# Performance work log

Measured on AMD Instinct MI355X. Metric: run time of the kernel, lower is better.

Reference implementation:

```python
import jax, jax.numpy as jnp
import numpy as np

B, S, DIM, H = 8, 1024, 1024, 16
HID = 512  # FeedForward default hidden_dim=512 (module passes only dim)
DH = DIM // H
EPS = 1e-5


def setup_inputs() -> dict:
    key = jax.random.key(0)
    ks = jax.random.split(key, 12)
    s = 1.0 / np.sqrt(DIM)
    return {
        "x": jax.random.normal(ks[0], (B, S, DIM), dtype=jnp.float32),
        "Wq": jax.random.normal(ks[1], (DIM, DIM), dtype=jnp.float32) * s,
        "Wk": jax.random.normal(ks[2], (DIM, DIM), dtype=jnp.float32) * s,
        "Wv": jax.random.normal(ks[3], (DIM, DIM), dtype=jnp.float32) * s,
        "Wo": jax.random.normal(ks[4], (DIM, DIM), dtype=jnp.float32) * s,
        "ln1_g": jnp.ones((DIM,), jnp.float32),
        "ln1_b": jnp.zeros((DIM,), jnp.float32),
        "W1": jax.random.normal(ks[5], (DIM, HID), dtype=jnp.float32) * s,
        "b1": jnp.zeros((HID,), jnp.float32),
        "W2": jax.random.normal(ks[6], (HID, DIM), dtype=jnp.float32) * (1.0 / np.sqrt(HID)),
        "b2": jnp.zeros((DIM,), jnp.float32),
        "ln2_g": jnp.ones((DIM,), jnp.float32),
        "ln2_b": jnp.zeros((DIM,), jnp.float32),
    }


def _layer_norm(x, g, b):
    mu = jnp.mean(x, axis=-1, keepdims=True)
    var = jnp.mean(jnp.square(x - mu), axis=-1, keepdims=True)
    return (x - mu) * jax.lax.rsqrt(var + EPS) * g + b


def reference(x, Wq, Wk, Wv, Wo, ln1_g, ln1_b, W1, b1, W2, b2, ln2_g, ln2_b):
    # Multi-head self-attention (dropout = identity at eval)
    def heads(t):  # [B,S,DIM] -> [B,H,S,DH]
        return t.reshape(B, S, H, DH).transpose(0, 2, 1, 3)

    q = heads(x @ Wq)
    k = heads(x @ Wk)
    v = heads(x @ Wv)
    scores = jnp.einsum("bhqd,bhkd->bhqk", q, k) / jnp.sqrt(jnp.float32(DH))
    attn = jax.nn.softmax(scores, axis=-1)
    ctx = jnp.einsum("bhqk,bhkd->bhqd", attn, v)
    ctx = ctx.transpose(0, 2, 1, 3).reshape(B, S, DIM)
    mha = ctx @ Wo

    h = _layer_norm(mha + x, ln1_g, ln1_b)
    ff = jax.nn.relu(h @ W1 + b1) @ W2 + b2
    out = _layer_norm(ff + h, ln2_g, ln2_b)
    return out
```

## Files before the change

### kernel.cpp

```cpp
#include <hip/hip_runtime.h>
#include <cstdint>
#include <cstddef>

#define DEV __device__ __forceinline__

typedef __bf16 bf16x8 __attribute__((ext_vector_type(8)));
typedef __bf16 bf16x4 __attribute__((ext_vector_type(4)));
typedef short  short4v __attribute__((ext_vector_type(4)));
typedef float  f32x4  __attribute__((ext_vector_type(4)));

static constexpr int Bb  = 8;
static constexpr int S   = 1024;
static constexpr int DIM = 1024;
static constexpr int H   = 16;
static constexpr int DH  = 64;
static constexpr int HID = 512;
static constexpr int M   = Bb * S;

DEV uint16_t f2bf(float f) {
  union { float f; uint32_t u; } v; v.f = f;
  uint32_t r = v.u + 0x7fffu + ((v.u >> 16) & 1u);
  return (uint16_t)(r >> 16);
}
DEV float bf2f(uint32_t u) {
  union { uint32_t u; float f; } v; v.u = u << 16;
  return v.f;
}

DEV void gl_lds16(const uint16_t* g, uint16_t* lds) {
  __builtin_amdgcn_global_load_lds(
      (const __attribute__((address_space(1))) void*)g,
      (__attribute__((address_space(3))) void*)lds, 16, 0, 0);
}

DEV bf16x8 ld8(const uint16_t* p) { return *reinterpret_cast<const bf16x8*>(p); }

#if __has_builtin(__builtin_amdgcn_mfma_f32_16x16x16bf16_1k)
DEV f32x4 mfma16(bf16x4 a, bf16x4 b, f32x4 c) {
  return __builtin_amdgcn_mfma_f32_16x16x16bf16_1k(
      __builtin_bit_cast(short4v, a), __builtin_bit_cast(short4v, b), c, 0, 0, 0);
}
#else
DEV f32x4 mfma16(bf16x4 a, bf16x4 b, f32x4 c) {
  asm volatile("v_mfma_f32_16x16x16_bf16 %0, %1, %2, %0" : "+v"(c) : "v"(a), "v"(b));
  return c;
}
#endif

DEV int swz(int row, int col) {
  return row * 64 + (((col >> 3) ^ (row & 7)) << 3) + (col & 7);
}

__global__ __launch_bounds__(256) void prep_all(const float* __restrict__ x,
                                                uint16_t* __restrict__ x16,
                                                const float* __restrict__ Wq,
                                                const float* __restrict__ Wk,
                                                const float* __restrict__ Wv,
                                                const float* __restrict__ Wo,
                                                const float* __restrict__ W1,
                                                const float* __restrict__ W2,
                                                uint16_t* __restrict__ wqkv_t,
                                                uint16_t* __restrict__ wo_t,
                                                uint16_t* __restrict__ w1_t,
                                                uint16_t* __restrict__ w2_t) {
  int bid = blockIdx.x;
  int tid = threadIdx.x;
  if (bid < 4096) {
    int i = (bid * 256 + tid) * 8;
    const float4* p = reinterpret_cast<const float4*>(x + i);
    float4 a = p[0], b = p[1];
    uint4 pk;
    pk.x = (uint32_t)f2bf(a.x) | ((uint32_t)f2bf(a.y) << 16);
    pk.y = (uint32_t)f2bf(a.z) | ((uint32_t)f2bf(a.w) << 16);
    pk.z = (uint32_t)f2bf(b.x) | ((uint32_t)f2bf(b.y) << 16);
    pk.w = (uint32_t)f2bf(b.z) | ((uint32_t)f2bf(b.w) << 16);
    *reinterpret_cast<uint4*>(x16 + i) = pk;
    return;
  }
  bid -= 4096;
  const float* src;
  uint16_t* dst;
  int R, C, bx, by;
  if (bid < 4096) {
    int which = bid >> 10, id = bid & 1023;
    if (which == 0)      { src = Wq; dst = wqkv_t; }
    else if (which == 1) { src = Wk; dst = wqkv_t + 1048576; }
    else if (which == 2) { src = Wv; dst = wqkv_t + 2097152; }
    else                 { src = Wo; dst = wo_t; }
    R = 1024; C = 1024; bx = id & 31; by = id >> 5;
  } else if (bid < 4608) {
    int id = bid - 4096;
    src = W1; dst = w1_t; R = 1024; C = 512; bx = id & 15; by = id >> 4;
  } else {
    int id = bid - 4608;
    src = W2; dst = w2_t; R = 512; C = 1024; bx = id & 31; by = id >> 5;
  }
  __shared__ float tile[32][33];
  int c0 = bx * 32, r0 = by * 32;
  int tx = tid & 31, ty = tid >> 5;
  #pragma unroll
  for (int i = 0; i < 4; i++)
    tile[ty + i * 8][tx] = src[(size_t)(r0 + ty + i * 8) * C + c0 + tx];
  __syncthreads();
  #pragma unroll
  for (int i = 0; i < 4; i++)
    dst[(size_t)(c0 + ty + i * 8) * R + r0 + tx] = f2bf(tile[tx][ty + i * 8]);
}

template <int BIAS, int RELU, int FUSEV>
__global__ __launch_bounds__(256) void gemm128p(const uint16_t* __restrict__ A,
                                                const uint16_t* __restrict__ Bt,
                                                const float* __restrict__ bias,
                                                uint16_t* __restrict__ Cout,
                                                uint16_t* __restrict__ vt,
                                                int N, int K) {
  __shared__ __align__(16) uint16_t As[2][128 * 64];
  __shared__ __align__(16) uint16_t Bs[2][128 * 64];
  const int tid = threadIdx.x;
  const int w = tid >> 6, l = tid & 63;
  const int hi = l >> 4, c = l & 15;
  int nwg = gridDim.x * gridDim.y;
  int lin = blockIdx.y * gridDim.x + blockIdx.x;
  if (!(nwg & 7)) lin = (lin & 7) * (nwg >> 3) + (lin >> 3);
  const int bx = lin % gridDim.x, by = lin / gridDim.x;
  const int m0 = by * 128, n0 = bx * 128;
  const int wr = (w >> 1) * 64, wc = (w & 1) * 64;
  const uint16_t* Ag = A + (size_t)m0 * K;
  const uint16_t* Bg = Bt + (size_t)n0 * K;
  f32x4 acc[4][4] = {};

  const int srow = tid >> 3;
  const int scol = ((tid & 7) ^ (srow & 7)) * 8;
  auto stage = [&](int k0, int buf) {
    #pragma unroll
    for (int i = 0; i < 4; i++)
      gl_lds16(Ag + (size_t)(i * 32 + srow) * K + k0 + scol,
               &As[buf][(i * 256 + w * 64) * 8]);
    #pragma unroll
    for (int i = 0; i < 4; i++)
      gl_lds16(Bg + (size_t)(i * 32 + srow) * K + k0 + scol,
               &Bs[buf][(i * 256 + w * 64) * 8]);
  };

  stage(0, 0);
  stage(64, 1);
  asm volatile("s_waitcnt vmcnt(8)" ::: "memory");
  __builtin_amdgcn_s_barrier();

  const int NTK = K >> 6;
  for (int t = 0; t < NTK; t++) {
    const int cur = t & 1;
    const uint16_t* Ab = As[cur];
    const uint16_t* Bb = Bs[cur];
    bf16x8 af[4][2], bfr[4][2];
    #pragma unroll
    for (int i = 0; i < 4; i++)
      #pragma unroll
      for (int kk = 0; kk < 2; kk++) {
        af[i][kk]  = ld8(&Ab[swz(wr + i * 16 + c, kk * 32 + hi * 8)]);
        bfr[i][kk] = ld8(&Bb[swz(wc + i * 16 + c, kk * 32 + hi * 8)]);
      }
    #pragma unroll
    for (int i = 0; i < 4; i++)
      #pragma unroll
      for (int j = 0; j < 4; j++) {
        acc[i][j] = __builtin_amdgcn_mfma_f32_16x16x32_bf16(af[i][0], bfr[j][0], acc[i][j], 0, 0, 0);
        acc[i][j] = __builtin_amdgcn_mfma_f32_16x16x32_bf16(af[i][1], bfr[j][1], acc[i][j], 0, 0, 0);
      }
    if (t == NTK - 1) break;
    asm volatile("s_waitcnt lgkmcnt(0)" ::: "memory");
    __builtin_amdgcn_s_barrier();
    if (t + 2 < NTK) {
      stage((t + 2) << 6, cur);
      asm volatile("s_waitcnt vmcnt(8)" ::: "memory");
    } else {
      asm volatile("s_waitcnt vmcnt(0)" ::: "memory");
    }
    __builtin_amdgcn_s_barrier();
  }

  const int r0 = m0 + wr + hi * 4;
  const int c0 = n0 + wc + c;
  if (FUSEV && c0 >= 2048) {
    #pragma unroll
    for (int j = 0; j < 4; j++) {
      int hd = c0 + j * 16 - 2048;
      #pragma unroll
      for (int i = 0; i < 4; i++) {
        int row = r0 + i * 16;
        size_t vi = ((size_t)(row >> 10) * 1024 + hd) * 1024 + (row & 1023);
        uint2 pk;
        pk.x = (uint32_t)f2bf(acc[i][j][0]) | ((uint32_t)f2bf(acc[i][j][1]) << 16);
        pk.y = (uint32_t)f2bf(acc[i][j][2]) | ((uint32_t)f2bf(acc[i][j][3]) << 16);
        *(uint2*)&vt[vi] = pk;
      }
    }
  } else {
    #pragma unroll
    for (int j = 0; j < 4; j++) {
      int col = c0 + j * 16;
      float bv = BIAS ? bias[col] : 0.0f;
      #pragma unroll
      for (int i = 0; i < 4; i++) {
        #pragma unroll
        for (int r = 0; r < 4; r++) {
          float v = acc[i][j][r] + bv;
          if (RELU) v = fmaxf(v, 0.0f);
          Cout[(size_t)(r0 + i * 16 + r) * N + col] = f2bf(v);
        }
      }
    }
  }
}

__global__ __launch_bounds__(256, 4) void attn9(const uint16_t* __restrict__ qkv,
                                                const uint16_t* __restrict__ vt,
                                                uint16_t* __restrict__ ctx) {
  int blk = blockIdx.x;
  int xcd = blk & 7, idx = blk >> 3;
  int qt = idx & 7;
  int bh = xcd + 8 * (idx >> 3);
  int h = bh & 15, b = bh >> 4;
  int q0 = qt * 128;
  int tid = threadIdx.x;
  int w = tid >> 6, l = tid & 63;
  int hi = l >> 4, c = l & 15;

  __shared__ __align__(16) uint16_t Klds[2][64 * 64];
  __shared__ __align__(16) uint16_t Vlds[2][64 * 64];

  const uint16_t* qbase = qkv + (size_t)(b * S + q0 + w * 32) * 3072 + h * 64;
  bf16x8 aq[2][2];
  #pragma unroll
  for (int qg = 0; qg < 2; qg++)
    #pragma unroll
    for (int dk = 0; dk < 2; dk++)
      aq[qg][dk] = ld8(qbase + (size_t)(qg * 16 + c) * 3072 + dk * 32 + hi * 8);

  f32x4 acc[2][4] = {};
  float psum[2] = {};

  const uint16_t* kgbase = qkv + (size_t)(b * S) * 3072 + 1024 + h * 64;
  const uint16_t* vgbase = vt + (size_t)(b * 16 + h) * 64 * S;

  const int lr = l >> 3, lc = l & 7;
  const int scol = (lc ^ lr) * 8;
  auto stage = [&](int kt, int buf) {
    #pragma unroll
    for (int i = 0; i < 2; i++) {
      int slab = w * 2 + i;
      gl_lds16(kgbase + (size_t)(kt + slab * 8 + lr) * 3072 + scol,
               &Klds[buf][slab * 512]);
      gl_lds16(vgbase + (size_t)(slab * 8 + lr) * S + kt + scol,
               &Vlds[buf][slab * 512]);
    }
  };

  stage(0, 0);
  asm volatile("s_waitcnt vmcnt(0)" ::: "memory");
  __syncthreads();

  constexpr float C2 = 0.125f * 1.44269504f;
  constexpr int NT = S / 64;
  for (int t = 0; t < NT; t++) {
    int cur = t & 1;
    if (t + 1 < NT) stage((t + 1) * 64, cur ^ 1);

    #pragma unroll
    for (int kb = 0; kb < 4; kb++) {
      bf16x8 kf0 = ld8(&Klds[cur][swz(kb * 16 + c, hi * 8)]);
      bf16x8 kf1 = ld8(&Klds[cur][swz(kb * 16 + c, 32 + hi * 8)]);
      bf16x4 pb[2];
      #pragma unroll
      for (int qg = 0; qg < 2; qg++) {
        f32x4 z = {0.f, 0.f, 0.f, 0.f};
        z = __builtin_amdgcn_mfma_f32_16x16x32_bf16(kf0, aq[qg][0], z, 0, 0, 0);
        z = __builtin_amdgcn_mfma_f32_16x16x32_bf16(kf1, aq[qg][1], z, 0, 0, 0);
        #pragma unroll
        for (int r = 0; r < 4; r++) {
          float p = exp2f(z[r] * C2);
          psum[qg] += p;
          pb[qg][r] = (__bf16)p;
        }
      }
      #pragma unroll
      for (int db = 0; db < 4; db++) {
        bf16x4 va = *(const bf16x4*)&Vlds[cur][swz(db * 16 + c, kb * 16 + hi * 4)];
        acc[0][db] = mfma16(va, pb[0], acc[0][db]);
        acc[1][db] = mfma16(va, pb[1], acc[1][db]);
      }
    }

    asm volatile("s_waitcnt vmcnt(0)" ::: "memory");
    __syncthreads();
  }

  #pragma unroll
  for (int qg = 0; qg < 2; qg++) {
    psum[qg] += __shfl_xor(psum[qg], 16);
    psum[qg] += __shfl_xor(psum[qg], 32);
  }

  uint16_t* Bw = &Vlds[w >> 1][(w & 1) * 2048];
  #pragma unroll
  for (int qg = 0; qg < 2; qg++) {
    float inv = 1.0f / psum[qg];
    int q = qg * 16 + c;
    #pragma unroll
    for (int db = 0; db < 4; db++) {
      uint2 pk;
      pk.x = (uint32_t)f2bf(acc[qg][db][0] * inv) |
             ((uint32_t)f2bf(acc[qg][db][1] * inv) << 16);
      pk.y = (uint32_t)f2bf(acc[qg][db][2] * inv) |
             ((uint32_t)f2bf(acc[qg][db][3] * inv) << 16);
      int chunk4 = (db * 4 + hi) ^ (q & 15);
      *(uint2*)&Bw[q * 64 + chunk4 * 4] = pk;
    }
  }
  int rrow = l >> 3, rch = l & 7;
  size_t gq0 = (size_t)(b * S + q0 + w * 32);
  #pragma unroll
  for (int it = 0; it < 4; it++) {
    int row = it * 8 + rrow;
    int k0 = (2 * rch) ^ (row & 15);
    int base = (k0 & ~1) * 4;
    uint4 v = *(const uint4*)&Bw[row * 64 + base];
    if (row & 1) { uint32_t t0 = v.x, t1 = v.y; v.x = v.z; v.y = v.w; v.z = t0; v.w = t1; }
    *(uint4*)&ctx[(gq0 + row) * DIM + h * 64 + rch * 8] = v;
  }
}

__global__ __launch_bounds__(256) void ln1_b(const uint16_t* __restrict__ a16,
                                             const uint16_t* __restrict__ x16,
                                             const float* __restrict__ g,
                                             const float* __restrict__ beta,
                                             uint16_t* __restrict__ h16) {
  int row = blockIdx.x;
  int t = threadIdx.x;
  int w = t >> 6, l = t & 63;
  uint2 av = reinterpret_cast<const uint2*>(a16 + (size_t)row * DIM)[t];
  uint2 xv = reinterpret_cast<const uint2*>(x16 + (size_t)row * DIM)[t];
  float v0 = bf2f(av.x & 0xffff) + bf2f(xv.x & 0xffff);
  float v1 = bf2f(av.x >> 16)    + bf2f(xv.x >> 16);
  float v2 = bf2f(av.y & 0xffff) + bf2f(xv.y & 0xffff);
  float v3 = bf2f(av.y >> 16)    + bf2f(xv.y >> 16);
  float s = v0 + v1 + v2 + v3;
  float sq = v0 * v0 + v1 * v1 + v2 * v2 + v3 * v3;
  #pragma unroll
  for (int off = 32; off >= 1; off >>= 1) {
    s += __shfl_xor(s, off);
    sq += __shfl_xor(sq, off);
  }
  __shared__ float ws[4], wq[4];
  if (l == 0) { ws[w] = s; wq[w] = sq; }
  __syncthreads();
  s = ws[0] + ws[1] + ws[2] + ws[3];
  sq = wq[0] + wq[1] + wq[2] + wq[3];
  float mu = s * (1.0f / DIM);
  float var = sq * (1.0f / DIM) - mu * mu;
  float rstd = rsqrtf(var + 1e-5f);
  const float4 gv = reinterpret_cast<const float4*>(g)[t];
  const float4 btv = reinterpret_cast<const float4*>(beta)[t];
  float o0 = (v0 - mu) * rstd * gv.x + btv.x;
  float o1 = (v1 - mu) * rstd * gv.y + btv.y;
  float o2 = (v2 - mu) * rstd * gv.z + btv.z;
  float o3 = (v3 - mu) * rstd * gv.w + btv.w;
  uint2 pk;
  pk.x = (uint32_t)f2bf(o0) | ((uint32_t)f2bf(o1) << 16);
  pk.y = (uint32_t)f2bf(o2) | ((uint32_t)f2bf(o3) << 16);
  reinterpret_cast<uint2*>(h16 + (size_t)row * DIM)[t] = pk;
}

__global__ __launch_bounds__(256) void ln2_b(const uint16_t* __restrict__ ff16,
                                             const uint16_t* __restrict__ h16,
                                             const float* __restrict__ g,
                                             const float* __restrict__ beta,
                                             float* __restrict__ out_f) {
  int row = blockIdx.x;
  int t = threadIdx.x;
  int w = t >> 6, l = t & 63;
  uint2 av = reinterpret_cast<const uint2*>(ff16 + (size_t)row * DIM)[t];
  uint2 hv = reinterpret_cast<const uint2*>(h16 + (size_t)row * DIM)[t];
  float v0 = bf2f(av.x & 0xffff) + bf2f(hv.x & 0xffff);
  float v1 = bf2f(av.x >> 16)    + bf2f(hv.x >> 16);
  float v2 = bf2f(av.y & 0xffff) + bf2f(hv.y & 0xffff);
  float v3 = bf2f(av.y >> 16)    + bf2f(hv.y >> 16);
  float s = v0 + v1 + v2 + v3;
  float sq = v0 * v0 + v1 * v1 + v2 * v2 + v3 * v3;
  #pragma unroll
  for (int off = 32; off >= 1; off >>= 1) {
    s += __shfl_xor(s, off);
    sq += __shfl_xor(sq, off);
  }
  __shared__ float ws[4], wq[4];
  if (l == 0) { ws[w] = s; wq[w] = sq; }
  __syncthreads();
  s = ws[0] + ws[1] + ws[2] + ws[3];
  sq = wq[0] + wq[1] + wq[2] + wq[3];
  float mu = s * (1.0f / DIM);
  float var = sq * (1.0f / DIM) - mu * mu;
  float rstd = rsqrtf(var + 1e-5f);
  const float4 gv = reinterpret_cast<const float4*>(g)[t];
  const float4 btv = reinterpret_cast<const float4*>(beta)[t];
  float4 o;
  o.x = (v0 - mu) * rstd * gv.x + btv.x;
  o.y = (v1 - mu) * rstd * gv.y + btv.y;
  o.z = (v2 - mu) * rstd * gv.z + btv.z;
  o.w = (v3 - mu) * rstd * gv.w + btv.w;
  reinterpret_cast<float4*>(out_f + (size_t)row * DIM)[t] = o;
}

extern "C" void kernel_launch(void* const* d_in, const int* in_sizes, int n_in,
                              void* d_out, int out_size, void* d_ws, size_t ws_size,
                              hipStream_t stream) {
  const float* x    = (const float*)d_in[0];
  const float* Wq   = (const float*)d_in[1];
  const float* Wk   = (const float*)d_in[2];
  const float* Wv   = (const float*)d_in[3];
  const float* Wo   = (const float*)d_in[4];
  const float* ln1g = (const float*)d_in[5];
  const float* ln1b = (const float*)d_in[6];
  const float* W1   = (const float*)d_in[7];
  const float* b1   = (const float*)d_in[8];
  const float* W2   = (const float*)d_in[9];
  const float* b2   = (const float*)d_in[10];
  const float* ln2g = (const float*)d_in[11];
  const float* ln2b = (const float*)d_in[12];
  float* out = (float*)d_out;

  char* ws = (char*)d_ws;
  uint16_t* wqkv_t = (uint16_t*)(ws + 0);
  uint16_t* wo_t   = (uint16_t*)(ws + 6291456);
  uint16_t* w1_t   = (uint16_t*)(ws + 8388608);
  uint16_t* w2_t   = (uint16_t*)(ws + 9437184);
  uint16_t* x16    = (uint16_t*)(ws + 10485760);
  uint16_t* qkv16  = (uint16_t*)(ws + 27262976);
  uint16_t* mha16  = (uint16_t*)(ws + 27262976);
  uint16_t* ff16   = (uint16_t*)(ws + 27262976);
  uint16_t* h16    = (uint16_t*)(ws + 60817408);
  uint16_t* vt16   = (uint16_t*)(ws + 77594624);
  uint16_t* mid16  = vt16;
  uint16_t* ctx16  = (uint16_t*)(ws + 94371840);

  prep_all<<<9216, 256, 0, stream>>>(x, x16, Wq, Wk, Wv, Wo, W1, W2,
                                     wqkv_t, wo_t, w1_t, w2_t);
  gemm128p<0, 0, 1><<<dim3(24, 64), 256, 0, stream>>>(x16, wqkv_t, nullptr,
                                                      qkv16, vt16, 3072, DIM);
  attn9<<<1024, 256, 0, stream>>>(qkv16, vt16, ctx16);
  gemm128p<0, 0, 0><<<dim3(8, 64), 256, 0, stream>>>(ctx16, wo_t, nullptr,
                                                     mha16, nullptr, DIM, DIM);
  ln1_b<<<M, 256, 0, stream>>>(mha16, x16, ln1g, ln1b, h16);
  gemm128p<1, 1, 0><<<dim3(4, 64), 256, 0, stream>>>(h16, w1_t, b1,
                                                     mid16, nullptr, HID, DIM);
  gemm128p<1, 0, 0><<<dim3(8, 64), 256, 0, stream>>>(mid16, w2_t, b2,
                                                     ff16, nullptr, DIM, HID);
  ln2_b<<<M, 256, 0, stream>>>(ff16, h16, ln2g, ln2b, out);
}
```

Measured before the change: 221.3 us.

## Triple-buffer attention K/V staging and restructure GEMM double-buffer prefetch

The attention kernel moves from double to triple buffering of K/V tiles in LDS. It prefetches two tiles ahead and waits with a partial vmcnt, so loads stay in flight across the barrier. The GEMM loop changes to issue the next tile's load at the top of each iteration, with a single full wait and barrier per step instead of two barriers and a two-ahead prefetch. The extra attention LDS (48KB) may reduce occupancy under the 4-block launch bound, and the GEMM change may expose more load latency.

```diff
diff --git a/kernel.cpp b/kernel.cpp
--- a/kernel.cpp
+++ b/kernel.cpp
@@ -143,13 +143,13 @@
   };
 
   stage(0, 0);
-  stage(64, 1);
-  asm volatile("s_waitcnt vmcnt(8)" ::: "memory");
+  asm volatile("s_waitcnt vmcnt(0)" ::: "memory");
   __builtin_amdgcn_s_barrier();
 
   const int NTK = K >> 6;
+  int cur = 0;
   for (int t = 0; t < NTK; t++) {
-    const int cur = t & 1;
+    if (t + 1 < NTK) stage((t + 1) << 6, cur ^ 1);
     const uint16_t* Ab = As[cur];
     const uint16_t* Bb = Bs[cur];
     bf16x8 af[4][2], bfr[4][2];
@@ -167,16 +167,11 @@
         acc[i][j] = __builtin_amdgcn_mfma_f32_16x16x32_bf16(af[i][0], bfr[j][0], acc[i][j], 0, 0, 0);
         acc[i][j] = __builtin_amdgcn_mfma_f32_16x16x32_bf16(af[i][1], bfr[j][1], acc[i][j], 0, 0, 0);
       }
-    if (t == NTK - 1) break;
-    asm volatile("s_waitcnt lgkmcnt(0)" ::: "memory");
-    __builtin_amdgcn_s_barrier();
-    if (t + 2 < NTK) {
-      stage((t + 2) << 6, cur);
-      asm volatile("s_waitcnt vmcnt(8)" ::: "memory");
-    } else {
+    if (t + 1 < NTK) {
       asm volatile("s_waitcnt vmcnt(0)" ::: "memory");
-    }
-    __builtin_amdgcn_s_barrier();
+      __builtin_amdgcn_s_barrier();
+    }
+    cur ^= 1;
   }
 
   const int r0 = m0 + wr + hi * 4;
@@ -213,9 +208,9 @@
   }
 }
 
-__global__ __launch_bounds__(256, 4) void attn9(const uint16_t* __restrict__ qkv,
-                                                const uint16_t* __restrict__ vt,
-                                                uint16_t* __restrict__ ctx) {
+__global__ __launch_bounds__(256, 4) void attn10(const uint16_t* __restrict__ qkv,
+                                                 const uint16_t* __restrict__ vt,
+                                                 uint16_t* __restrict__ ctx) {
   int blk = blockIdx.x;
   int xcd = blk & 7, idx = blk >> 3;
   int qt = idx & 7;
@@ -226,8 +221,8 @@
   int w = tid >> 6, l = tid & 63;
   int hi = l >> 4, c = l & 15;
 
-  __shared__ __align__(16) uint16_t Klds[2][64 * 64];
-  __shared__ __align__(16) uint16_t Vlds[2][64 * 64];
+  __shared__ __align__(16) uint16_t Klds[3][64 * 64];
+  __shared__ __align__(16) uint16_t Vlds[3][64 * 64];
 
   const uint16_t* qbase = qkv + (size_t)(b * S + q0 + w * 32) * 3072 + h * 64;
   bf16x8 aq[2][2];
@@ -257,19 +252,25 @@
   };
 
   stage(0, 0);
-  asm volatile("s_waitcnt vmcnt(0)" ::: "memory");
+  stage(64, 1);
+  asm volatile("s_waitcnt vmcnt(4)" ::: "memory");
   __syncthreads();
 
   constexpr float C2 = 0.125f * 1.44269504f;
   constexpr int NT = S / 64;
+  int cur = 0;
   for (int t = 0; t < NT; t++) {
-    int cur = t & 1;
-    if (t + 1 < NT) stage((t + 1) * 64, cur ^ 1);
+    if (t + 2 < NT) {
+      int nnx = cur + 2; if (nnx >= 3) nnx -= 3;
+      stage((t + 2) * 64, nnx);
+    }
+    const uint16_t* Kc = Klds[cur];
+    const uint16_t* Vc = Vlds[cur];
 
     #pragma unroll
     for (int kb = 0; kb < 4; kb++) {
-      bf16x8 kf0 = ld8(&Klds[cur][swz(kb * 16 + c, hi * 8)]);
-      bf16x8 kf1 = ld8(&Klds[cur][swz(kb * 16 + c, 32 + hi * 8)]);
+      bf16x8 kf0 = ld8(&Kc[swz(kb * 16 + c, hi * 8)]);
+      bf16x8 kf1 = ld8(&Kc[swz(kb * 16 + c, 32 + hi * 8)]);
       bf16x4 pb[2];
       #pragma unroll
       for (int qg = 0; qg < 2; qg++) {
@@ -285,14 +286,19 @@
       }
       #pragma unroll
       for (int db = 0; db < 4; db++) {
-        bf16x4 va = *(const bf16x4*)&Vlds[cur][swz(db * 16 + c, kb * 16 + hi * 4)];
+        bf16x4 va = *(const bf16x4*)&Vc[swz(db * 16 + c, kb * 16 + hi * 4)];
         acc[0][db] = mfma16(va, pb[0], acc[0][db]);
         acc[1][db] = mfma16(va, pb[1], acc[1][db]);
       }
     }
 
-    asm volatile("s_waitcnt vmcnt(0)" ::: "memory");
+    if (t + 2 < NT) {
+      asm volatile("s_waitcnt vmcnt(4)" ::: "memory");
+    } else {
+      asm volatile("s_waitcnt vmcnt(0)" ::: "memory");
+    }
     __syncthreads();
+    cur = cur + 1; if (cur == 3) cur = 0;
   }
 
   #pragma unroll
@@ -301,7 +307,7 @@
     psum[qg] += __shfl_xor(psum[qg], 32);
   }
 
-  uint16_t* Bw = &Vlds[w >> 1][(w & 1) * 2048];
+  uint16_t* Bw = &Vlds[0][w * 2048];
   #pragma unroll
   for (int qg = 0; qg < 2; qg++) {
     float inv = 1.0f / psum[qg];
@@ -446,7 +452,7 @@
                                      wqkv_t, wo_t, w1_t, w2_t);
   gemm128p<0, 0, 1><<<dim3(24, 64), 256, 0, stream>>>(x16, wqkv_t, nullptr,
                                                       qkv16, vt16, 3072, DIM);
-  attn9<<<1024, 256, 0, stream>>>(qkv16, vt16, ctx16);
+  attn10<<<1024, 256, 0, stream>>>(qkv16, vt16, ctx16);
   gemm128p<0, 0, 0><<<dim3(8, 64), 256, 0, stream>>>(ctx16, wo_t, nullptr,
                                                      mha16, nullptr, DIM, DIM);
   ln1_b<<<M, 256, 0, stream>>>(mha16, x16, ln1g, ln1b, h16);
```

Result: slower. 230.0 us (+4.0%).
